# Kernel tuning notes

Hardware: AMD Instinct MI355X
Metric: run time of the kernel (lower is better)

Reference implementation:

```python
import jax, jax.numpy as jnp
import numpy as np

NC = 6            # CPAB tessellation cells (tess_size=6, zero_boundary=True)
DIM = NC - 1      # theta dimension = 5
SIG_LEN = 2048
CHANNELS = 3
BATCH = 256
FC_IN = 64 * 168  # flattened net_part1 output for signal_len=2048
NUM_SCALING = 0   # N in transform_data_ss
EPS_BN = 1e-5


def _cpab_basis():
    """QR null-space basis of the CPAB continuity + zero-boundary constraints.
    Params ordered [a_1,b_1,...,a_NC,b_NC]; v(x)=a_c x + b_c on cell c."""
    nc = NC
    L = np.zeros((nc + 1, 2 * nc))
    for k in range(1, nc):  # continuity at internal knots x_k = k/nc
        xk = k / nc
        L[k - 1, 2 * (k - 1)] = xk
        L[k - 1, 2 * (k - 1) + 1] = 1.0
        L[k - 1, 2 * k] = -xk
        L[k - 1, 2 * k + 1] = -1.0
    L[nc - 1, 1] = 1.0        # v(0) = 0  -> b_1 = 0
    L[nc, 2 * (nc - 1)] = 1.0  # v(1) = 0 -> a_nc + b_nc = 0
    L[nc, 2 * nc - 1] = 1.0
    Q, _ = np.linalg.qr(L.T, mode='complete')
    return np.ascontiguousarray(Q[:, nc + 1:]).astype(np.float32)  # (12, 5)


def _conv1d(x, w, b):
    y = jax.lax.conv_general_dilated(x, w, (1,), 'VALID',
                                     dimension_numbers=('NCH', 'OIH', 'NCH'))
    return y + b[None, :, None]


def _maxpool1d(x, k, s):
    return jax.lax.reduce_window(x, -jnp.inf, jax.lax.max, (1, 1, k), (1, 1, s), 'VALID')


def _bn(x, g, b, m, v):  # eval-mode BatchNorm1d
    return (x - m[None, :, None]) * (g / jnp.sqrt(v + EPS_BN))[None, :, None] + b[None, :, None]


def _integrate(x, A):
    """Exact CPAB 1D flow integration over t=1 with cell-crossing handling.
    x: (B, n) points in [0,1]; A: (B, NC, 2) per-cell (a, b). Monotone
    trajectories cross at most NC-1 boundaries -> fixed NC+1 iterations."""
    a_all, b_all = A[:, :, 0], A[:, :, 1]
    t = jnp.ones_like(x)
    for _ in range(NC + 1):
        c = jnp.clip(jnp.floor(x * NC).astype(jnp.int32), 0, NC - 1)
        a = jnp.take_along_axis(a_all, c, axis=1)
        b = jnp.take_along_axis(b_all, c, axis=1)
        v = a * x + b
        xb = jnp.where(v >= 0, (c + 1).astype(x.dtype) / NC, c.astype(x.dtype) / NC)
        big_a = jnp.abs(a) > 1e-8
        a_s = jnp.where(big_a, a, 1.0)
        z = x + b / a_s        # shifted coord: x(t) = z*exp(a t) - b/a
        zb = xb + b / a_s
        ratio = zb / jnp.where(jnp.abs(z) > 1e-12, z, 1e-12)
        t_exp = jnp.log(jnp.maximum(ratio, 1e-12)) / a_s
        v_s = jnp.where(jnp.abs(v) > 1e-12, v, 1.0)
        t_lin = (xb - x) / v_s
        thit = jnp.where(big_a, t_exp, t_lin)
        valid = (jnp.abs(v) > 1e-12) & (thit > 0) & (jnp.where(big_a, ratio, 1.0) > 0)
        thit = jnp.where(valid, thit, jnp.inf)
        tau = jnp.minimum(t, thit)
        x_new = jnp.where(big_a, z * jnp.exp(a * tau) - (z - x), x + b * tau)
        hit = thit <= t
        nudge = jnp.where(v >= 0, 1e-6, -1e-6)  # push into next cell
        x = jnp.clip(jnp.where(hit, xb + nudge, x_new), 0.0, 1.0)
        t = jnp.maximum(t - tau, 0.0)
    return x


def _interp1d(data, pos):
    """data: (B, L, C); pos: (B, n) in [0,1] -> (B, n, C) linear interpolation."""
    Lw = data.shape[1]
    p = jnp.clip(pos, 0.0, 1.0) * (Lw - 1)
    x0 = jnp.clip(jnp.floor(p).astype(jnp.int32), 0, Lw - 2)
    w = (p - x0.astype(p.dtype))[:, :, None]
    d0 = jnp.take_along_axis(data, x0[:, :, None], axis=1)
    d1 = jnp.take_along_axis(data, (x0 + 1)[:, :, None], axis=1)
    return d0 * (1.0 - w) + d1 * w


def _transform_data_ss(data, theta, basis, outsize, N):
    """CPAB scaling-and-squaring warp of data (B, L, C) by theta (B, DIM)."""
    Bsz = theta.shape[0]
    A = (theta @ basis.T).reshape(Bsz, NC, 2) / (2.0 ** N)
    grid = jnp.linspace(0.0, 1.0, outsize, dtype=data.dtype)
    grid_t = _integrate(jnp.broadcast_to(grid, (Bsz, outsize)), A)
    for _ in range(N):  # squaring: compose the warp with itself
        grid_t = _interp1d(grid_t[:, :, None], grid_t)[:, :, 0]
    return _interp1d(data, grid_t)


def reference(x, conv1_w, conv1_b, bn1_g, bn1_b, bn1_m, bn1_v,
              conv2_w, conv2_b, bn2_g, bn2_b, bn2_m, bn2_v,
              conv3_w, conv3_b, bn3_g, bn3_b, bn3_m, bn3_v,
              fc1_w, fc1_b, fc2_w, fc2_b, fc3_w, fc3_b, fc4_w, fc4_b, basis):
    # localization net (n_recurrence = 1, back_version = True)
    h = jax.nn.relu(_maxpool1d(_bn(_conv1d(x, conv1_w, conv1_b), bn1_g, bn1_b, bn1_m, bn1_v), 3, 2))
    h = jax.nn.relu(_maxpool1d(_bn(_conv1d(h, conv2_w, conv2_b), bn2_g, bn2_b, bn2_m, bn2_v), 3, 3))
    h = jax.nn.relu(_maxpool1d(_bn(_conv1d(h, conv3_w, conv3_b), bn3_g, bn3_b, bn3_m, bn3_v), 3, 2))
    xs = h.reshape(h.shape[0], -1)  # (B, 64*168)
    xs = jax.nn.relu(xs @ fc1_w.T + fc1_b)
    xs = jax.nn.relu(xs @ fc2_w.T + fc2_b)
    xs = jax.nn.relu(xs @ fc3_w.T + fc3_b)
    theta = jnp.tanh(xs @ fc4_w.T + fc4_b)  # (B, 5)
    data = jnp.transpose(x, (0, 2, 1))       # (B, L, C)
    warped = _transform_data_ss(data, theta, basis, SIG_LEN, NUM_SCALING)
    return jnp.transpose(warped, (0, 2, 1))  # (B, C, L)


def setup_inputs() -> dict:
    key = jax.random.key(0)
    ks = jax.random.split(key, 16)
    def nrm(k, shape, scale):
        return (jax.random.normal(k, shape) * scale).astype(jnp.float32)
    inp = {}
    inp['x'] = jax.random.normal(ks[0], (BATCH, CHANNELS, SIG_LEN), dtype=jnp.float32)
    inp['conv1_w'] = nrm(ks[1], (128, CHANNELS, 3), (CHANNELS * 3) ** -0.5)
    inp['conv1_b'] = nrm(ks[2], (128,), 0.01)
    inp['bn1_g'] = jnp.ones((128,), jnp.float32)
    inp['bn1_b'] = jnp.zeros((128,), jnp.float32)
    inp['bn1_m'] = nrm(ks[3], (128,), 0.1)
    inp['bn1_v'] = jnp.ones((128,), jnp.float32)
    inp['conv2_w'] = nrm(ks[4], (64, 128, 5), (128 * 5) ** -0.5)
    inp['conv2_b'] = nrm(ks[5], (64,), 0.01)
    inp['bn2_g'] = jnp.ones((64,), jnp.float32)
    inp['bn2_b'] = jnp.zeros((64,), jnp.float32)
    inp['bn2_m'] = nrm(ks[6], (64,), 0.1)
    inp['bn2_v'] = jnp.ones((64,), jnp.float32)
    inp['conv3_w'] = nrm(ks[7], (64, 64, 3), (64 * 3) ** -0.5)
    inp['conv3_b'] = nrm(ks[8], (64,), 0.01)
    inp['bn3_g'] = jnp.ones((64,), jnp.float32)
    inp['bn3_b'] = jnp.zeros((64,), jnp.float32)
    inp['bn3_m'] = nrm(ks[9], (64,), 0.1)
    inp['bn3_v'] = jnp.ones((64,), jnp.float32)
    inp['fc1_w'] = nrm(ks[10], (48, FC_IN), FC_IN ** -0.5)
    inp['fc1_b'] = jnp.zeros((48,), jnp.float32)
    inp['fc2_w'] = nrm(ks[11], (32, 48), 48 ** -0.5)
    inp['fc2_b'] = jnp.zeros((32,), jnp.float32)
    inp['fc3_w'] = nrm(ks[12], (16, 32), 32 ** -0.5)
    inp['fc3_b'] = jnp.zeros((16,), jnp.float32)
    # near-identity warp head (original zero-inits weight, identity bias)
    inp['fc4_w'] = nrm(ks[13], (DIM, 16), 0.01)
    inp['fc4_b'] = nrm(ks[14], (DIM,), 0.01)
    inp['basis'] = jnp.asarray(_cpab_basis())
    return inp
```

## Files before the change

kernel.cpp:

```cpp
#include <hip/hip_runtime.h>
#include <math.h>

#define BATCH   256
#define SIGLEN  2048
#define L1OUT   1022
#define L2OUT   339
#define L3OUT   168
#define FCIN    10752

#define TP2   16
#define NROW  52
#define H1S   136
#define H1SZ  (NROW*H1S)

#define H3R   346

typedef float f32x2  __attribute__((ext_vector_type(2)));
typedef float f32x4  __attribute__((ext_vector_type(4)));
typedef short s16x8  __attribute__((ext_vector_type(8)));

__device__ __forceinline__ unsigned short f2bf(float f) {
    unsigned int u = __float_as_uint(f);
    return (unsigned short)((u + 0x7fffu + ((u >> 16) & 1u)) >> 16);
}
__device__ __forceinline__ float bf2f(unsigned short h) {
    return __uint_as_float(((unsigned int)h) << 16);
}
__device__ __forceinline__ f32x2 pkfma(f32x2 a, f32x2 b, f32x2 c) {
    f32x2 d;
    asm("v_pk_fma_f32 %0, %1, %2, %3" : "=v"(d) : "v"(a), "v"(b), "v"(c));
    return d;
}

__launch_bounds__(256)
__global__ void prep_kernel(
    const float* __restrict__ conv1_b,
    const float* __restrict__ g1, const float* __restrict__ b1,
    const float* __restrict__ m1, const float* __restrict__ v1,
    const float* __restrict__ conv2_w, const float* __restrict__ conv2_b,
    const float* __restrict__ g2, const float* __restrict__ b2,
    const float* __restrict__ m2, const float* __restrict__ v2,
    const float* __restrict__ conv3_w, const float* __restrict__ conv3_b,
    const float* __restrict__ g3, const float* __restrict__ b3,
    const float* __restrict__ m3, const float* __restrict__ v3,
    const float* __restrict__ fc1_w,
    unsigned short* __restrict__ w2hi, unsigned short* __restrict__ w2lo,
    unsigned short* __restrict__ w3hi, unsigned short* __restrict__ w3lo,
    float* __restrict__ wp1,
    float* __restrict__ so1, float* __restrict__ so2, float* __restrict__ so3)
{
    __shared__ float tl[64 * 169];

    int t   = threadIdx.x;
    int tid = blockIdx.x * 256 + t;

    if (blockIdx.x < 48) {
        int o = blockIdx.x;
        for (int i4 = 4*t; i4 < FCIN; i4 += 1024) {
            int co = i4 / L3OUT, u = i4 - co * L3OUT;
            float4 v = *(const float4*)(fc1_w + o*FCIN + i4);
            tl[co*169 + u    ] = v.x;
            tl[co*169 + u + 1] = v.y;
            tl[co*169 + u + 2] = v.z;
            tl[co*169 + u + 3] = v.w;
        }
        __syncthreads();
        for (int i4 = 4*t; i4 < FCIN; i4 += 1024) {
            int u = i4 >> 6, co = i4 & 63;
            float4 v;
            v.x = tl[(co    )*169 + u];
            v.y = tl[(co + 1)*169 + u];
            v.z = tl[(co + 2)*169 + u];
            v.w = tl[(co + 3)*169 + u];
            *(float4*)(wp1 + o*FCIN + i4) = v;
        }
    }

    {
        int i = tid - 16384;
        if ((unsigned)i < 40960u) {
            int co = i / 640; int rr = i - co*640; int ci = rr / 5; int k = rr - ci*5;
            float w = conv2_w[i];
            unsigned short hi = f2bf(w);
            unsigned short lo = f2bf(w - bf2f(hi));
            int dst = ((k*4 + (ci >> 5))*64 + co)*32 + (ci & 31);
            w2hi[dst] = hi;
            w2lo[dst] = lo;
        }
    }
    {
        int i = tid - 57344;
        if ((unsigned)i < 12288u) {
            int co = i / 192; int r = i - co*192; int ci = r / 3; int k = r - ci*3;
            float w = conv3_w[i];
            unsigned short hi = f2bf(w);
            unsigned short lo = f2bf(w - bf2f(hi));
            int dst = ((k*2 + (ci >> 5))*64 + co)*32 + (ci & 31);
            w3hi[dst] = hi;
            w3lo[dst] = lo;
        }
    }
    {
        int i = tid - 69632;
        if ((unsigned)i < 128u) {
            float s = g1[i] / sqrtf(v1[i] + 1e-5f);
            so1[i]       = s;
            so1[128 + i] = (conv1_b[i] - m1[i]) * s + b1[i];
        }
        int i2 = tid - 69888;
        if ((unsigned)i2 < 64u) {
            float s2 = g2[i2] / sqrtf(v2[i2] + 1e-5f);
            so2[i2]      = s2;
            so2[64 + i2] = (conv2_b[i2] - m2[i2]) * s2 + b2[i2];
            float s3 = g3[i2] / sqrtf(v3[i2] + 1e-5f);
            so3[i2]      = s3;
            so3[64 + i2] = (conv3_b[i2] - m3[i2]) * s3 + b3[i2];
        }
    }
}

__launch_bounds__(256, 5)
__global__ void conv12_kernel(
    const float* __restrict__ x, const float* __restrict__ w1,
    const unsigned short* __restrict__ w2hi, const unsigned short* __restrict__ w2lo,
    const float* __restrict__ so1, const float* __restrict__ so2,
    unsigned int* __restrict__ h2p)
{
    __shared__ unsigned short h1hi[H1SZ];
    __shared__ unsigned short h1lo[H1SZ];

    int t  = threadIdx.x;
    int b  = blockIdx.x;
    int u0 = blockIdx.y * TP2;
    int q0 = 3 * u0;
    int wv = __builtin_amdgcn_readfirstlane(t >> 6);
    int l  = t & 63;
    int m  = l & 15;
    int qd = l >> 4;

    {
        f32x2 wp[9], s1p, o1p;
        const float* wa = w1 + (2*l)*9;
        #pragma unroll
        for (int j = 0; j < 9; ++j) wp[j] = (f32x2){wa[j], wa[9 + j]};
        s1p = (f32x2){so1[2*l], so1[2*l + 1]};
        o1p = (f32x2){so1[128 + 2*l], so1[128 + 2*l + 1]};

        int rbase = 13 * wv;
        int W0 = 2*(q0 + rbase);
        const float* xp0 = x + b*3*SIGLEN;

        f32x2 xb[3][6];
        if (W0 + 5 <= SIGLEN - 1) {
            #pragma unroll
            for (int ci = 0; ci < 3; ++ci) {
                const float* xp = xp0 + ci*SIGLEN + W0;
                float2 v01 = *(const float2*)(xp);
                float2 v23 = *(const float2*)(xp + 2);
                float2 v45 = *(const float2*)(xp + 4);
                xb[ci][0] = (f32x2){v01.x, v01.x};
                xb[ci][1] = (f32x2){v01.y, v01.y};
                xb[ci][2] = (f32x2){v23.x, v23.x};
                xb[ci][3] = (f32x2){v23.y, v23.y};
                xb[ci][4] = (f32x2){v45.x, v45.x};
                xb[ci][5] = (f32x2){v45.y, v45.y};
            }
        } else {
            #pragma unroll
            for (int ci = 0; ci < 3; ++ci)
                #pragma unroll
                for (int j = 0; j < 6; ++j) {
                    int xi = W0 + j; xi = xi < SIGLEN ? xi : SIGLEN - 1;
                    float v = xp0[ci*SIGLEN + xi];
                    xb[ci][j] = (f32x2){v, v};
                }
        }

        f32x2 cr = (f32x2){0.f, 0.f};
        #pragma unroll
        for (int s = 0; s < 13; ++s) {
            int r = rbase + s;
            f32x2 r1 = (f32x2){0.f, 0.f}, r2 = (f32x2){0.f, 0.f};
            #pragma unroll
            for (int ci = 0; ci < 3; ++ci) {
                #pragma unroll
                for (int tp = 0; tp < 3; ++tp) {
                    r1 = pkfma(xb[ci][1 + tp], wp[ci*3 + tp], r1);
                    r2 = pkfma(xb[ci][2 + tp], wp[ci*3 + tp], r2);
                }
            }
            f32x2 r0;
            if (s == 0) {
                r0 = (f32x2){0.f, 0.f};
                #pragma unroll
                for (int ci = 0; ci < 3; ++ci)
                    #pragma unroll
                    for (int tp = 0; tp < 3; ++tp)
                        r0 = pkfma(xb[ci][tp], wp[ci*3 + tp], r0);
            } else {
                r0 = cr;
            }
            cr = r2;

            float m0 = fmaxf(r0[0], fmaxf(r1[0], r2[0]));
            float m1 = fmaxf(r0[1], fmaxf(r1[1], r2[1]));
            float v0 = fmaxf(fmaf(s1p[0], m0, o1p[0]), 0.f);
            float v1 = fmaxf(fmaf(s1p[1], m1, o1p[1]), 0.f);

            unsigned ua = __float_as_uint(v0);
            unsigned ub = __float_as_uint(v1);
            unsigned hipack = __builtin_amdgcn_perm(ub, ua, 0x07060302u);
            float ra = v0 - __uint_as_float(ua & 0xffff0000u);
            float rb = v1 - __uint_as_float(ub & 0xffff0000u);
            unsigned lopack = __builtin_amdgcn_perm(__float_as_uint(rb), __float_as_uint(ra),
                                                    0x07060302u);
            ((unsigned*)h1hi)[r*68 + l] = hipack;
            ((unsigned*)h1lo)[r*68 + l] = lopack;

            if (s < 12) {
                #pragma unroll
                for (int ci = 0; ci < 3; ++ci) {
                    xb[ci][0] = xb[ci][2]; xb[ci][1] = xb[ci][3];
                    xb[ci][2] = xb[ci][4]; xb[ci][3] = xb[ci][5];
                }
                int Wn = W0 + 2*s + 6;
                if (Wn + 1 <= SIGLEN - 1) {
                    #pragma unroll
                    for (int ci = 0; ci < 3; ++ci) {
                        float2 v = *(const float2*)(xp0 + ci*SIGLEN + Wn);
                        xb[ci][4] = (f32x2){v.x, v.x};
                        xb[ci][5] = (f32x2){v.y, v.y};
                    }
                } else {
                    #pragma unroll
                    for (int ci = 0; ci < 3; ++ci) {
                        int x4 = Wn     < SIGLEN ? Wn     : SIGLEN - 1;
                        int x5 = Wn + 1 < SIGLEN ? Wn + 1 : SIGLEN - 1;
                        float a4 = xp0[ci*SIGLEN + x4];
                        float a5 = xp0[ci*SIGLEN + x5];
                        xb[ci][4] = (f32x2){a4, a4};
                        xb[ci][5] = (f32x2){a5, a5};
                    }
                }
            }
        }
    }
    __syncthreads();

    f32x4 acc[3] = {(f32x4)(0.f), (f32x4)(0.f), (f32x4)(0.f)};

    const unsigned short* whb = w2hi + wv*512 + m*32 + qd*8;
    const unsigned short* wlb = w2lo + wv*512 + m*32 + qd*8;

    for (int k = 0; k < 5; ++k) {
        #pragma unroll
        for (int cb = 0; cb < 4; ++cb) {
            int st = k*4 + cb;
            s16x8 wh = *(const s16x8*)(whb + st*2048);
            s16x8 wl = *(const s16x8*)(wlb + st*2048);
            #pragma unroll
            for (int pt = 0; pt < 3; ++pt) {
                int row = pt*16 + m + k;
                s16x8 ah = *(const s16x8*)&h1hi[row*H1S + cb*32 + qd*8];
                s16x8 al = *(const s16x8*)&h1lo[row*H1S + cb*32 + qd*8];
                acc[pt] = __builtin_amdgcn_mfma_f32_16x16x32_bf16(ah, wh, acc[pt], 0, 0, 0);
                acc[pt] = __builtin_amdgcn_mfma_f32_16x16x32_bf16(al, wh, acc[pt], 0, 0, 0);
                acc[pt] = __builtin_amdgcn_mfma_f32_16x16x32_bf16(ah, wl, acc[pt], 0, 0, 0);
            }
        }
    }
    __syncthreads();

    float* c2 = (float*)h1hi;
    #pragma unroll
    for (int pt = 0; pt < 3; ++pt)
        #pragma unroll
        for (int rg = 0; rg < 4; ++rg)
            c2[(pt*16 + qd*4 + rg)*65 + wv*16 + m] = acc[pt][rg];
    __syncthreads();

    #pragma unroll
    for (int it = 0; it < 4; ++it) {
        int idx = t + it*256;
        int ul = idx >> 6, co = idx & 63;
        int u = u0 + ul;
        if (u < L2OUT) {
            float v0 = c2[(3*ul  )*65 + co];
            float v1 = c2[(3*ul+1)*65 + co];
            float v2 = c2[(3*ul+2)*65 + co];
            float mm = fmaxf(v0, fmaxf(v1, v2));
            float v  = fmaxf(fmaf(so2[co], mm, so2[64 + co]), 0.f);
            unsigned uu = __float_as_uint(v);
            float rr = v - __uint_as_float(uu & 0xffff0000u);
            h2p[(b*L2OUT + u)*64 + co] = (uu >> 16) | (__float_as_uint(rr) & 0xffff0000u);
        }
    }
}

__launch_bounds__(1024, 1)
__global__ void tail_kernel(
    const unsigned int* __restrict__ h2p,
    const unsigned short* __restrict__ w3hi, const unsigned short* __restrict__ w3lo,
    const float* __restrict__ so3, const float* __restrict__ wp1,
    const float* __restrict__ fc1_b,
    const float* __restrict__ fc2_w, const float* __restrict__ fc2_b,
    const float* __restrict__ fc3_w, const float* __restrict__ fc3_b,
    const float* __restrict__ fc4_w, const float* __restrict__ fc4_b,
    const float* __restrict__ basis,
    const float* __restrict__ x,
    float* __restrict__ out)
{
    __shared__ unsigned short h3s[2*H3R*72];
    __shared__ float c3buf[64*65];
    __shared__ float pools[28*64];
    __shared__ float xsr[48];
    __shared__ float xs48[48], hl[32], gl[16], thl[5], Al[12];

    int t  = threadIdx.x;
    int b  = blockIdx.x;
    int wv = __builtin_amdgcn_readfirstlane(t >> 6);
    int l  = t & 63;
    int m  = l & 15;
    int qd = l >> 4;
    int pt = wv >> 2;
    int c4 = wv & 3;

    {
        const unsigned int* src = h2p + (b*L2OUT)*64;
        unsigned* dhi = (unsigned*)h3s;
        unsigned* dlo = (unsigned*)(h3s + H3R*72);
        for (int i = t; i < H3R*32; i += 1024) {
            int r = i >> 5, cp = i & 31;
            int g = r > (L2OUT-1) ? (L2OUT-1) : r;
            uint2 v = ((const uint2*)src)[g*32 + cp];
            dhi[r*36 + cp] = __builtin_amdgcn_perm(v.y, v.x, 0x05040100u);
            dlo[r*36 + cp] = __builtin_amdgcn_perm(v.y, v.x, 0x07060302u);
        }
    }

    s16x8 wh[6], wl[6];
    #pragma unroll
    for (int s = 0; s < 6; ++s) {
        wh[s] = *(const s16x8*)(w3hi + s*2048 + (c4*16 + m)*32 + qd*8);
        wl[s] = *(const s16x8*)(w3lo + s*2048 + (c4*16 + m)*32 + qd*8);
    }

    __syncthreads();

    int o0 = wv * 3;
    int ug  = l >> 4;
    int co4 = (l & 15) * 4;
    float fa[3] = {0.f, 0.f, 0.f};

    for (int ti = 0; ti < 6; ++ti) {
        int u0 = ti * 28;

        f32x4 acc = (f32x4)(0.f);
        #pragma unroll
        for (int s = 0; s < 6; ++s) {
            int row = 2*u0 + pt*16 + m + (s >> 1);
            int off = (s & 1)*32 + qd*8;
            s16x8 ah = *(const s16x8*)&h3s[row*72 + off];
            s16x8 al = *(const s16x8*)&h3s[H3R*72 + row*72 + off];
            acc = __builtin_amdgcn_mfma_f32_16x16x32_bf16(ah, wh[s], acc, 0, 0, 0);
            acc = __builtin_amdgcn_mfma_f32_16x16x32_bf16(al, wh[s], acc, 0, 0, 0);
            acc = __builtin_amdgcn_mfma_f32_16x16x32_bf16(ah, wl[s], acc, 0, 0, 0);
        }
        __syncthreads();

        #pragma unroll
        for (int rg = 0; rg < 4; ++rg)
            c3buf[(pt*16 + qd*4 + rg)*65 + c4*16 + m] = acc[rg];
        __syncthreads();

        #pragma unroll
        for (int k = 0; k < 2; ++k) {
            int idx = t + k*1024;
            if (idx < 28*64) {
                int u = idx >> 6, co = idx & 63;
                int p = 2*u;
                float v0 = c3buf[(p  )*65 + co];
                float v1 = c3buf[(p+1)*65 + co];
                float v2 = c3buf[(p+2)*65 + co];
                pools[idx] = fmaxf(fmaf(so3[co], fmaxf(v0, fmaxf(v1, v2)), so3[64 + co]), 0.f);
            }
        }
        __syncthreads();

        #pragma unroll
        for (int uu = 0; uu < 7; ++uu) {
            int u = 4*uu + ug;
            f32x4 p = *(const f32x4*)&pools[u*64 + co4];
            const float* wb = wp1 + (u0 + u)*64 + co4;
            #pragma unroll
            for (int j = 0; j < 3; ++j) {
                f32x4 w = *(const f32x4*)(wb + (o0 + j)*FCIN);
                fa[j] = fmaf(p[0], w[0], fmaf(p[1], w[1], fmaf(p[2], w[2], fmaf(p[3], w[3], fa[j]))));
            }
        }
    }

    #pragma unroll
    for (int j = 0; j < 3; ++j) {
        #pragma unroll
        for (int off = 32; off > 0; off >>= 1)
            fa[j] += __shfl_xor(fa[j], off, 64);
    }
    if (l == 0) {
        #pragma unroll
        for (int j = 0; j < 3; ++j) xsr[o0 + j] = fa[j];
    }
    __syncthreads();

    if (t < 48) xs48[t] = fmaxf(xsr[t] + fc1_b[t], 0.f);
    __syncthreads();
    if (t < 32) {
        float sv = fc2_b[t];
        #pragma unroll
        for (int k = 0; k < 48; ++k) sv = fmaf(fc2_w[t * 48 + k], xs48[k], sv);
        hl[t] = fmaxf(sv, 0.f);
    }
    __syncthreads();
    if (t < 16) {
        float sv = fc3_b[t];
        #pragma unroll
        for (int k = 0; k < 32; ++k) sv = fmaf(fc3_w[t * 32 + k], hl[k], sv);
        gl[t] = fmaxf(sv, 0.f);
    }
    __syncthreads();
    if (t < 5) {
        float sv = fc4_b[t];
        #pragma unroll
        for (int k = 0; k < 16; ++k) sv = fmaf(fc4_w[t * 16 + k], gl[k], sv);
        thl[t] = tanhf(sv);
    }
    __syncthreads();
    if (t < 12) {
        float sv = 0.f;
        #pragma unroll
        for (int d = 0; d < 5; ++d) sv = fmaf(basis[t * 5 + d], thl[d], sv);
        Al[t] = sv;
    }
    __syncthreads();

    float a_r[6], b_r[6];
    #pragma unroll
    for (int c = 0; c < 6; ++c) { a_r[c] = Al[2*c]; b_r[c] = Al[2*c+1]; }

    #pragma unroll
    for (int cc = 0; cc < 2; ++cc) {
        int i = cc * 1024 + t;
        float xp = (float)i / 2047.f;
        float tt = 1.f;
        for (int it = 0; it < 7; ++it) {
            int c = (int)floorf(xp * 6.f);
            c = min(max(c, 0), 5);
            float a  = a_r[c], bb = b_r[c];
            float v  = a * xp + bb;
            float xb = (v >= 0.f) ? (float)(c + 1) / 6.f : (float)c / 6.f;
            bool  big_a = fabsf(a) > 1e-8f;
            float a_s = big_a ? a : 1.f;
            float z   = xp + bb / a_s;
            float zb  = xb + bb / a_s;
            float zden = (fabsf(z) > 1e-12f) ? z : 1e-12f;
            float ratio = zb / zden;
            float t_exp = logf(fmaxf(ratio, 1e-12f)) / a_s;
            float v_s   = (fabsf(v) > 1e-12f) ? v : 1.f;
            float t_lin = (xb - xp) / v_s;
            float thit  = big_a ? t_exp : t_lin;
            bool valid  = (fabsf(v) > 1e-12f) && (thit > 0.f) && ((big_a ? ratio : 1.f) > 0.f);
            if (!valid) thit = __builtin_inff();
            float tau   = fminf(tt, thit);
            float x_new = big_a ? (z * expf(a * tau) - (z - xp)) : (xp + bb * tau);
            bool hit    = (thit <= tt);
            float nudge = (v >= 0.f) ? 1e-6f : -1e-6f;
            xp = hit ? (xb + nudge) : x_new;
            xp = fminf(fmaxf(xp, 0.f), 1.f);
            tt = fmaxf(tt - tau, 0.f);
        }
        float p = fminf(fmaxf(xp, 0.f), 1.f) * 2047.f;
        int i0 = (int)floorf(p);
        i0 = min(max(i0, 0), 2046);
        float w = p - (float)i0;
        #pragma unroll
        for (int c = 0; c < 3; ++c) {
            const float* d = &x[(b * 3 + c) * SIGLEN];
            out[(b * 3 + c) * SIGLEN + i] = d[i0] * (1.f - w) + d[i0 + 1] * w;
        }
    }
}

extern "C" void kernel_launch(void* const* d_in, const int* in_sizes, int n_in,
                              void* d_out, int out_size, void* d_ws, size_t ws_size,
                              hipStream_t stream) {
    (void)in_sizes; (void)n_in; (void)out_size; (void)ws_size;
    const float* x       = (const float*)d_in[0];
    const float* conv1_w = (const float*)d_in[1];
    const float* conv1_b = (const float*)d_in[2];
    const float* bn1_g   = (const float*)d_in[3];
    const float* bn1_b   = (const float*)d_in[4];
    const float* bn1_m   = (const float*)d_in[5];
    const float* bn1_v   = (const float*)d_in[6];
    const float* conv2_w = (const float*)d_in[7];
    const float* conv2_b = (const float*)d_in[8];
    const float* bn2_g   = (const float*)d_in[9];
    const float* bn2_b   = (const float*)d_in[10];
    const float* bn2_m   = (const float*)d_in[11];
    const float* bn2_v   = (const float*)d_in[12];
    const float* conv3_w = (const float*)d_in[13];
    const float* conv3_b = (const float*)d_in[14];
    const float* bn3_g   = (const float*)d_in[15];
    const float* bn3_b   = (const float*)d_in[16];
    const float* bn3_m   = (const float*)d_in[17];
    const float* bn3_v   = (const float*)d_in[18];
    const float* fc1_w   = (const float*)d_in[19];
    const float* fc1_b   = (const float*)d_in[20];
    const float* fc2_w   = (const float*)d_in[21];
    const float* fc2_b   = (const float*)d_in[22];
    const float* fc3_w   = (const float*)d_in[23];
    const float* fc3_b   = (const float*)d_in[24];
    const float* fc4_w   = (const float*)d_in[25];
    const float* fc4_b   = (const float*)d_in[26];
    const float* basis   = (const float*)d_in[27];

    unsigned short* w2hi = (unsigned short*)d_ws;
    unsigned short* w2lo = w2hi + 40960;
    unsigned short* w3hi = w2lo + 40960;
    unsigned short* w3lo = w3hi + 12288;
    float* ws   = (float*)d_ws;
    float* so1  = ws + 53248;
    float* so2  = so1 + 256;
    float* so3  = so2 + 128;
    float* wp1  = so3 + 128;
    unsigned int* h2p = (unsigned int*)(wp1 + 516096);

    prep_kernel<<<512, 256, 0, stream>>>(
        conv1_b, bn1_g, bn1_b, bn1_m, bn1_v,
        conv2_w, conv2_b, bn2_g, bn2_b, bn2_m, bn2_v,
        conv3_w, conv3_b, bn3_g, bn3_b, bn3_m, bn3_v,
        fc1_w, w2hi, w2lo, w3hi, w3lo, wp1, so1, so2, so3);

    dim3 g2(BATCH, (L2OUT + TP2 - 1) / TP2);
    conv12_kernel<<<g2, 256, 0, stream>>>(x, conv1_w, w2hi, w2lo, so1, so2, h2p);

    tail_kernel<<<BATCH, 1024, 0, stream>>>(h2p, w3hi, w3lo, so3, wp1,
                                            fc1_b, fc2_w, fc2_b, fc3_w, fc3_b,
                                            fc4_w, fc4_b, basis, x, (float*)d_out);
}
```

Measured before the change: 245.1 us.

## Read fc1 weights in native layout in tail kernel, drop prep transpose

The per-call transpose of fc1_w into a channel-interleaved wp1 buffer is removed from the prep kernel. The tail kernel now reads fc1_w in its original (co, u) layout, with one lane per channel and float4 loads along u. The pools reads become scalar per-lane LDS reads, and the BN scale and shift values are hoisted into registers. This saves about 2 MB of global write plus read and shrinks the prep grid, but the fc1 loads in the tail now stride L3OUT floats across lanes, so they are less coalesced.

```diff
diff --git a/kernel.cpp b/kernel.cpp
--- a/kernel.cpp
+++ b/kernel.cpp
@@ -43,53 +43,24 @@
     const float* __restrict__ conv3_w, const float* __restrict__ conv3_b,
     const float* __restrict__ g3, const float* __restrict__ b3,
     const float* __restrict__ m3, const float* __restrict__ v3,
-    const float* __restrict__ fc1_w,
     unsigned short* __restrict__ w2hi, unsigned short* __restrict__ w2lo,
     unsigned short* __restrict__ w3hi, unsigned short* __restrict__ w3lo,
-    float* __restrict__ wp1,
     float* __restrict__ so1, float* __restrict__ so2, float* __restrict__ so3)
 {
-    __shared__ float tl[64 * 169];
-
-    int t   = threadIdx.x;
-    int tid = blockIdx.x * 256 + t;
-
-    if (blockIdx.x < 48) {
-        int o = blockIdx.x;
-        for (int i4 = 4*t; i4 < FCIN; i4 += 1024) {
-            int co = i4 / L3OUT, u = i4 - co * L3OUT;
-            float4 v = *(const float4*)(fc1_w + o*FCIN + i4);
-            tl[co*169 + u    ] = v.x;
-            tl[co*169 + u + 1] = v.y;
-            tl[co*169 + u + 2] = v.z;
-            tl[co*169 + u + 3] = v.w;
-        }
-        __syncthreads();
-        for (int i4 = 4*t; i4 < FCIN; i4 += 1024) {
-            int u = i4 >> 6, co = i4 & 63;
-            float4 v;
-            v.x = tl[(co    )*169 + u];
-            v.y = tl[(co + 1)*169 + u];
-            v.z = tl[(co + 2)*169 + u];
-            v.w = tl[(co + 3)*169 + u];
-            *(float4*)(wp1 + o*FCIN + i4) = v;
-        }
-    }
-
+    int tid = blockIdx.x * 256 + threadIdx.x;
+
+    if (tid < 40960) {
+        int i = tid;
+        int co = i / 640; int rr = i - co*640; int ci = rr / 5; int k = rr - ci*5;
+        float w = conv2_w[i];
+        unsigned short hi = f2bf(w);
+        unsigned short lo = f2bf(w - bf2f(hi));
+        int dst = ((k*4 + (ci >> 5))*64 + co)*32 + (ci & 31);
+        w2hi[dst] = hi;
+        w2lo[dst] = lo;
+    }
     {
-        int i = tid - 16384;
-        if ((unsigned)i < 40960u) {
-            int co = i / 640; int rr = i - co*640; int ci = rr / 5; int k = rr - ci*5;
-            float w = conv2_w[i];
-            unsigned short hi = f2bf(w);
-            unsigned short lo = f2bf(w - bf2f(hi));
-            int dst = ((k*4 + (ci >> 5))*64 + co)*32 + (ci & 31);
-            w2hi[dst] = hi;
-            w2lo[dst] = lo;
-        }
-    }
-    {
-        int i = tid - 57344;
+        int i = tid - 40960;
         if ((unsigned)i < 12288u) {
             int co = i / 192; int r = i - co*192; int ci = r / 3; int k = r - ci*3;
             float w = conv3_w[i];
@@ -101,13 +72,13 @@
         }
     }
     {
-        int i = tid - 69632;
+        int i = tid - 53248;
         if ((unsigned)i < 128u) {
             float s = g1[i] / sqrtf(v1[i] + 1e-5f);
             so1[i]       = s;
             so1[128 + i] = (conv1_b[i] - m1[i]) * s + b1[i];
         }
-        int i2 = tid - 69888;
+        int i2 = tid - 53376;
         if ((unsigned)i2 < 64u) {
             float s2 = g2[i2] / sqrtf(v2[i2] + 1e-5f);
             so2[i2]      = s2;
@@ -301,7 +272,7 @@
 __global__ void tail_kernel(
     const unsigned int* __restrict__ h2p,
     const unsigned short* __restrict__ w3hi, const unsigned short* __restrict__ w3lo,
-    const float* __restrict__ so3, const float* __restrict__ wp1,
+    const float* __restrict__ so3, const float* __restrict__ fc1_w,
     const float* __restrict__ fc1_b,
     const float* __restrict__ fc2_w, const float* __restrict__ fc2_b,
     const float* __restrict__ fc3_w, const float* __restrict__ fc3_b,
@@ -344,12 +315,11 @@
         wh[s] = *(const s16x8*)(w3hi + s*2048 + (c4*16 + m)*32 + qd*8);
         wl[s] = *(const s16x8*)(w3lo + s*2048 + (c4*16 + m)*32 + qd*8);
     }
+    float s3v = so3[l], o3v = so3[64 + l];
 
     __syncthreads();
 
     int o0 = wv * 3;
-    int ug  = l >> 4;
-    int co4 = (l & 15) * 4;
     float fa[3] = {0.f, 0.f, 0.f};
 
     for (int ti = 0; ti < 6; ++ti) {
@@ -382,20 +352,23 @@
                 float v0 = c3buf[(p  )*65 + co];
                 float v1 = c3buf[(p+1)*65 + co];
                 float v2 = c3buf[(p+2)*65 + co];
-                pools[idx] = fmaxf(fmaf(so3[co], fmaxf(v0, fmaxf(v1, v2)), so3[64 + co]), 0.f);
+                pools[idx] = fmaxf(fmaf(s3v, fmaxf(v0, fmaxf(v1, v2)), o3v), 0.f);
             }
         }
         __syncthreads();
 
+        const float* wb0 = fc1_w + l*L3OUT + u0;
         #pragma unroll
         for (int uu = 0; uu < 7; ++uu) {
-            int u = 4*uu + ug;
-            f32x4 p = *(const f32x4*)&pools[u*64 + co4];
-            const float* wb = wp1 + (u0 + u)*64 + co4;
+            int ub = 4*uu;
+            float p0 = pools[(ub  )*64 + l];
+            float p1 = pools[(ub+1)*64 + l];
+            float p2 = pools[(ub+2)*64 + l];
+            float p3 = pools[(ub+3)*64 + l];
             #pragma unroll
             for (int j = 0; j < 3; ++j) {
-                f32x4 w = *(const f32x4*)(wb + (o0 + j)*FCIN);
-                fa[j] = fmaf(p[0], w[0], fmaf(p[1], w[1], fmaf(p[2], w[2], fmaf(p[3], w[3], fa[j]))));
+                float4 w = *(const float4*)(wb0 + (o0 + j)*FCIN + ub);
+                fa[j] = fmaf(p0, w.x, fmaf(p1, w.y, fmaf(p2, w.z, fmaf(p3, w.w, fa[j]))));
             }
         }
     }
@@ -531,19 +504,18 @@
     float* so1  = ws + 53248;
     float* so2  = so1 + 256;
     float* so3  = so2 + 128;
-    float* wp1  = so3 + 128;
-    unsigned int* h2p = (unsigned int*)(wp1 + 516096);
-
-    prep_kernel<<<512, 256, 0, stream>>>(
+    unsigned int* h2p = (unsigned int*)(so3 + 128);
+
+    prep_kernel<<<256, 256, 0, stream>>>(
         conv1_b, bn1_g, bn1_b, bn1_m, bn1_v,
         conv2_w, conv2_b, bn2_g, bn2_b, bn2_m, bn2_v,
         conv3_w, conv3_b, bn3_g, bn3_b, bn3_m, bn3_v,
-        fc1_w, w2hi, w2lo, w3hi, w3lo, wp1, so1, so2, so3);
+        w2hi, w2lo, w3hi, w3lo, so1, so2, so3);
 
     dim3 g2(BATCH, (L2OUT + TP2 - 1) / TP2);
     conv12_kernel<<<g2, 256, 0, stream>>>(x, conv1_w, w2hi, w2lo, so1, so2, h2p);
 
-    tail_kernel<<<BATCH, 1024, 0, stream>>>(h2p, w3hi, w3lo, so3, wp1,
+    tail_kernel<<<BATCH, 1024, 0, stream>>>(h2p, w3hi, w3lo, so3, fc1_w,
                                             fc1_b, fc2_w, fc2_b, fc3_w, fc3_b,
                                             fc4_w, fc4_b, basis, x, (float*)d_out);
 }
```

After: 280.5 us. 14.4% more time.
